# Optimization experiments

Hardware: AMD Instinct MI355X
Metric: run time of the kernel (lower is better)

Reference implementation:

```python
import jax, jax.numpy as jnp
import numpy as np
from jax import lax

B, A, H, W = 64, 8, 64, 128
T_EXP = 32
ACTION_HORIZON = 64
DS = 1.0          # reward_cfg['ds']
TEMPERATURE = 0.1 # policy_kwargs['temperature'], method='sharpen'
FOV_HALF_ANGLE_DEG = 35.0
FOV_MAX_RANGE = 100


def _build_buffers():
    # per-action 3x3 one-hot transition kernels: weight 1.0 at 'center' cell,
    # 0.0 at left/right cells (as in MaxEntIRL.__init__ with policy_method='pp')
    center = [[2, 2], [2, 1], [2, 0], [1, 2], [1, 0], [0, 2], [0, 1], [0, 0]]
    tp = np.zeros((A, 1, 3, 3), np.float32)
    for i, (r, c) in enumerate(center):
        tp[i, 0, r, c] = 1.0
    # trapezoidal FOV mask built on a (2H, W) grid, then cropped to first H rows
    rows = np.arange(2 * H, dtype=np.float32)[:, None]
    cols = np.arange(W, dtype=np.float32)[None, :]
    half = np.tan(np.deg2rad(FOV_HALF_ANGLE_DEG)) * rows
    mask = ((np.abs(cols - (W - 1) / 2.0) <= half) & (rows <= FOV_MAX_RANGE))
    fov = mask.astype(np.float32)[:H][None, None]  # (1,1,H,W)
    dyn = np.array([[-1, -1], [-1, 0], [-1, 1], [0, -1],
                    [0, 1], [1, -1], [1, 0], [1, 1]], np.int32)
    return jnp.asarray(tp), jnp.asarray(fov), jnp.asarray(dyn)


def setup_inputs() -> dict:
    key = jax.random.key(0)
    k1, k2 = jax.random.split(key)
    policy = jax.random.normal(k1, (B, A, H, W), jnp.float32)
    # expert SE(2)-like poses; only [:, :, :2, 2] translations are read.
    # Scale to [0,100) so grid cells spread over the map before clamping.
    expert = jax.random.uniform(k2, (B, T_EXP, 3, 3), jnp.float32) * 100.0
    tp, fov, dyn = _build_buffers()
    return {"policy": policy, "expert": expert, "transition_probs": tp,
            "fov_mask": fov, "dynamics": dyn, "action_horizon": ACTION_HORIZON}


def reference(policy, expert, transition_probs, fov_mask, dynamics, action_horizon):
    Bn, An, Hn, Wn = policy.shape
    n_states = Hn * Wn
    barange = jnp.arange(Bn)

    # expert poses -> clamped grid cells  (S: (B, T, 2))
    S = jnp.floor_divide(expert[:, :, :2, 2], DS).astype(jnp.int32)
    S = jnp.stack([jnp.clip(S[..., 0], 0, Hn - 1),
                   jnp.clip(S[..., 1], 0, Wn - 1)], axis=-1)

    # earliest pose inside FOV (argmax of bool gives first True, else 0)
    mask2d = fov_mask[0, 0]
    in_fov = mask2d[S[..., 0], S[..., 1]] > 0  # (B, T)
    idx0 = jnp.argmax(in_fov, axis=1)
    S0c = S[barange, idx0]     # (B, 2) start cell
    S1c = S[:, -1]             # (B, 2) terminal cell
    S0 = S0c[:, 0] * Wn + S0c[:, 1]
    S1 = S1c[:, 0] * Wn + S1c[:, 1]

    # sharpen policy over action dim (stable softmax with temperature)
    logits = (policy - jnp.max(policy, axis=1, keepdims=True)) / TEMPERATURE
    policy_2d = jax.nn.softmax(logits, axis=1)  # (B, A, H, W)

    mu0 = jnp.zeros((Bn, n_states), jnp.float32).at[barange, S0].set(1.0)

    def step(carry, _):
        prev, total = carry
        # zero_terminal_state: kill visitation mass at the terminal cell
        prev_z = prev.at[barange, S1].set(0.0)
        pm = policy_2d * prev_z.reshape(Bn, 1, Hn, Wn)  # (B, A, H, W)
        new = lax.conv_general_dilated(
            pm, transition_probs, window_strides=(1, 1),
            padding=[(1, 1), (1, 1)],
            dimension_numbers=("NCHW", "OIHW", "NCHW"),
            feature_group_count=An)
        new = jnp.sum(new, axis=1).reshape(Bn, n_states)
        return (new, total + prev_z), None

    (last, total), _ = lax.scan(step, (mu0, jnp.zeros_like(mu0)),
                                None, length=action_horizon - 1)
    mu = (total + last).reshape(Bn, Hn, Wn)

    # greedy rollout (torch runs this under no_grad)
    policy_flat = policy.reshape(Bn, An, n_states)
    most_likely_action = jnp.argmax(policy_flat, axis=1)  # (B, n_states)
    most_likely_action = lax.stop_gradient(most_likely_action)

    def roll(St, _):
        a = most_likely_action[barange, St]
        coord = jnp.stack([St // Wn, St % Wn], axis=1) + dynamics[a]
        coord = jnp.stack([jnp.clip(coord[:, 0], 0, Hn - 1),
                           jnp.clip(coord[:, 1], 0, Wn - 1)], axis=1)
        return coord[:, 0] * Wn + coord[:, 1], coord

    _, coords = lax.scan(roll, S0, None, length=action_horizon - 1)  # (T-1,B,2)
    states = jnp.concatenate([S0c[None].astype(coords.dtype), coords],
                             axis=0).transpose(1, 0, 2)  # (B, T, 2)
    bidx = jnp.broadcast_to(barange[:, None], (Bn, action_horizon))
    states_grid = jnp.zeros((Bn, Hn, Wn), jnp.float32).at[
        bidx, states[..., 0], states[..., 1]].add(1.0)
    return mu, states_grid, states
```

## Files before the change

### kernel.cpp

```cpp
#include <hip/hip_runtime.h>

#define THREADS 1024

typedef unsigned int u32;
typedef unsigned long long u64;

constexpr int BN = 64, AN = 8, HN = 64, WN = 128;
constexpr int HWN = HN * WN;
constexpr int TEXP = 32, AH = 64;
constexpr size_t LDS_BYTES = (size_t)AN * HWN * 2;

constexpr int GYc[8] = { 1, 1, 1, 0, 0, -1, -1, -1 };
constexpr int GXc[8] = { 1, 0, -1, 1, -1, 1, 0, -1 };

typedef _Float16 h2 __attribute__((ext_vector_type(2)));
union U { u32 u; h2 p; _Float16 h[2]; };

__device__ __forceinline__ h2  H(u32 x) { U t; t.u = x; return t.p; }
__device__ __forceinline__ u32 Bc(h2 x) { U t; t.p = x; return t.u; }

__device__ __forceinline__ u32 ab16(u32 hi, u32 lo) {
    return (u32)((((u64)hi << 32) | lo) >> 16);
}
__device__ __forceinline__ u32 wsr1(u32 x) {
    return (u32)__builtin_amdgcn_update_dpp(0, (int)x, 0x138, 0xf, 0xf, true);
}
__device__ __forceinline__ u32 wsl1(u32 x) {
    return (u32)__builtin_amdgcn_update_dpp(0, (int)x, 0x130, 0xf, 0xf, true);
}
__device__ __forceinline__ u32 shL(u32 d) { return ab16(d, wsr1(d)); }
__device__ __forceinline__ u32 shR(u32 d) { return ab16(wsl1(d), d); }

extern "C" __global__ __launch_bounds__(THREADS)
void maxent_fused(const float* __restrict__ policy,
                  const float* __restrict__ expert,
                  const float* __restrict__ fovm,
                  const int*   __restrict__ dyn,
                  float* __restrict__ out)
{
    (void)dyn;
    extern __shared__ char smem[];
    const int tid  = threadIdx.x;
    const int lane = tid & 63;
    const bool isScan = blockIdx.x < BN;
    const int b = isScan ? (int)blockIdx.x : (int)blockIdx.x - BN;

    int Sr = 0, Sc = 0; bool infov = false;
    if (lane < TEXP) {
        float e0 = expert[b * (TEXP * 9) + lane * 9 + 2];
        float e1 = expert[b * (TEXP * 9) + lane * 9 + 5];
        int r = (int)floorf(e0); r = r < 0 ? 0 : (r > HN - 1 ? HN - 1 : r);
        int c = (int)floorf(e1); c = c < 0 ? 0 : (c > WN - 1 ? WN - 1 : c);
        Sr = r; Sc = c;
        infov = fovm[r * WN + c] > 0.0f;
    }
    unsigned long long fmask = __ballot(infov);
    int idx0 = fmask ? (__ffsll(fmask) - 1) : 0;
    const int S0r = __shfl(Sr, idx0), S0c = __shfl(Sc, idx0);
    const int S1r = __shfl(Sr, TEXP - 1), S1c = __shfl(Sc, TEXP - 1);
    const bool S0eqS1 = (S0r == S1r) && (S0c == S1c);

    if (isScan) {
        _Float16* Pl = (_Float16*)smem;

        const float* pb = policy + (size_t)b * AN * HWN;
        #pragma unroll
        for (int kk = 0; kk < 2; ++kk) {
            const int pix = (kk * THREADS + tid) * 4;
            float v[8][4];
            float m[4] = {-3.4e38f, -3.4e38f, -3.4e38f, -3.4e38f};
            #pragma unroll
            for (int a = 0; a < 8; ++a) {
                float4 f = *(const float4*)(pb + a * HWN + pix);
                v[a][0] = f.x; v[a][1] = f.y; v[a][2] = f.z; v[a][3] = f.w;
                m[0] = fmaxf(m[0], f.x); m[1] = fmaxf(m[1], f.y);
                m[2] = fmaxf(m[2], f.z); m[3] = fmaxf(m[3], f.w);
            }
            float s[4] = {0.f, 0.f, 0.f, 0.f};
            #pragma unroll
            for (int a = 0; a < 8; ++a)
                #pragma unroll
                for (int j = 0; j < 4; ++j) { v[a][j] = __expf((v[a][j] - m[j]) * 10.0f); s[j] += v[a][j]; }
            float inv[4];
            #pragma unroll
            for (int j = 0; j < 4; ++j) inv[j] = 1.0f / s[j];
            #pragma unroll
            for (int a = 0; a < 8; ++a) {
                u32 lo = (u32)__builtin_bit_cast(unsigned short, (_Float16)(v[a][0] * inv[0]))
                       | ((u32)__builtin_bit_cast(unsigned short, (_Float16)(v[a][1] * inv[1])) << 16);
                u32 hi = (u32)__builtin_bit_cast(unsigned short, (_Float16)(v[a][2] * inv[2]))
                       | ((u32)__builtin_bit_cast(unsigned short, (_Float16)(v[a][3] * inv[3])) << 16);
                uint2 pk2; pk2.x = lo; pk2.y = hi;
                *(uint2*)(Pl + a * HWN + pix) = pk2;
            }
        }
        __syncthreads();

        const int w = tid >> 6;
        const int rbase = 4 * w;

        u32 pa[8][4];
        #pragma unroll
        for (int a = 0; a < 8; ++a) {
            const int gy = GYc[a], gx = GXc[a];
            #pragma unroll
            for (int r = 0; r < 4; ++r) {
                const int sr = rbase + r + gy;
                u32 d = 0;
                if (sr >= 0 && sr < HN)
                    d = *(const u32*)(Pl + a * HWN + sr * WN + 2 * lane);
                pa[a][r] = (gx == 0) ? d : ((gx == 1) ? shR(d) : shL(d));
            }
        }
        __syncthreads();

        u32* hx  = (u32*)smem;
        u32* flg = hx + 4096;
        for (int i = tid; i < 4096 + 256; i += THREADS) hx[i] = 0;

        u32 x[6], zm[4];
        #pragma unroll
        for (int r = 0; r < 4; ++r) {
            const int gr = rbase + r;
            x[1 + r] = (!S0eqS1 && gr == S0r && (S0c >> 1) == lane)
                         ? ((S0c & 1) ? 0x3C000000u : 0x00003C00u) : 0u;
            zm[r] = ~0u;
            if (gr == S1r && (S1c >> 1) == lane)
                zm[r] = (S1c & 1) ? 0x0000FFFFu : 0xFFFF0000u;
        }
        x[0] = 0; x[5] = 0;

        int t0 = rbase - S0r; { int t1 = S0r - (rbase + 3); if (t1 > t0) t0 = t1; }
        const int t_act = (t0 > 1) ? (t0 - 1) : 0;

        __syncthreads();
        hx[(2 * w + 0) * 64 + lane] = x[1];
        hx[(2 * w + 1) * 64 + lane] = x[4];
        if (lane == 0) flg[w * 16] = (u32)t_act;
        __syncthreads();

        u32 t16[4], nn[4];
        float tot[8];
        #pragma unroll
        for (int r = 0; r < 4; ++r) { t16[r] = 0; nn[r] = 0; }
        #pragma unroll
        for (int k = 0; k < 8; ++k) tot[k] = 0.f;

        const int rdT = (2 * w - 1) * 64 + lane;
        const int rdD = (2 * w + 2) * 64 + lane;
        const int wr0 = (2 * w + 0) * 64 + lane;
        const int wr3 = (2 * w + 1) * 64 + lane;
        u32* fL = flg + (w - 1) * 16;
        u32* fR = flg + (w + 1) * 16;
        u32* fme = flg + w * 16;

        for (int it = t_act; it < AH - 1; ++it) {
            const int pb_ = (it & 1) << 11;
            const int wb_ = 2048 - pb_;

            if (w > 0)
                while (__hip_atomic_load(fL, __ATOMIC_ACQUIRE, __HIP_MEMORY_SCOPE_WORKGROUP) < (u32)it)
                    __builtin_amdgcn_s_sleep(1);
            if (w < 15)
                while (__hip_atomic_load(fR, __ATOMIC_ACQUIRE, __HIP_MEMORY_SCOPE_WORKGROUP) < (u32)it)
                    __builtin_amdgcn_s_sleep(1);

            const u32 hT = (w > 0)  ? hx[pb_ + rdT] : 0u;
            const u32 hD = (w < 15) ? hx[pb_ + rdD] : 0u;

            #pragma unroll
            for (int r = 0; r < 4; ++r) t16[r] = Bc(H(t16[r]) + H(x[1 + r]));

            u32 L[6], R[6];
            #pragma unroll
            for (int i = 1; i <= 4; ++i) { L[i] = shL(x[i]); R[i] = shR(x[i]); }

            u32 ns[4];
            constexpr int RO[4] = {1, 2, 0, 3};
            #pragma unroll
            for (int ri = 0; ri < 4; ++ri) {
                const int r = RO[ri];
                const u32 cm1 = (r == 0) ? hT      : x[r];
                const u32 lm1 = (r == 0) ? shL(hT) : L[r];
                const u32 rm1 = (r == 0) ? shR(hT) : R[r];
                const u32 cp1 = (r == 3) ? hD      : x[r + 2];
                const u32 lp1 = (r == 3) ? shL(hD) : L[r + 2];
                const u32 rp1 = (r == 3) ? shR(hD) : R[r + 2];
                h2 acc0 =  H(pa[0][r]) * H(rp1);
                acc0 += H(pa[1][r]) * H(cp1);
                acc0 += H(pa[2][r]) * H(lp1);
                acc0 += H(pa[3][r]) * H(R[r + 1]);
                h2 acc1 =  H(pa[4][r]) * H(L[r + 1]);
                acc1 += H(pa[5][r]) * H(rm1);
                acc1 += H(pa[6][r]) * H(cm1);
                acc1 += H(pa[7][r]) * H(lm1);
                const u32 un = Bc(acc0 + acc1);
                nn[r] = un;
                ns[r] = un & zm[r];
            }
            #pragma unroll
            for (int r = 0; r < 4; ++r) x[1 + r] = ns[r];

            hx[wb_ + wr0] = x[1];
            hx[wb_ + wr3] = x[4];
            __hip_atomic_store(fme, (u32)(it + 1), __ATOMIC_RELEASE, __HIP_MEMORY_SCOPE_WORKGROUP);

            if ((it & 3) == 3 || it == AH - 2) {
                #pragma unroll
                for (int r = 0; r < 4; ++r) {
                    tot[2*r]   += (float)H(t16[r]).x;
                    tot[2*r+1] += (float)H(t16[r]).y;
                    t16[r] = 0;
                }
            }
        }

        #pragma unroll
        for (int r = 0; r < 4; ++r) {
            float2 f;
            f.x = tot[2*r]   + (float)H(nn[r]).x;
            f.y = tot[2*r+1] + (float)H(nn[r]).y;
            *(float2*)(out + (size_t)b * HWN + (rbase + r) * WN + 2 * lane) = f;
        }

    } else {
        short* amap = (short*)smem;
        float* grid = (float*)(smem + 16384);
        const float* pb = policy + (size_t)b * AN * HWN;
        #pragma unroll
        for (int c = 0; c < 2; ++c) {
            const int pix = (c * THREADS + tid) * 4;
            float4 f0 = *(const float4*)(pb + pix);
            float b0 = f0.x, b1 = f0.y, b2 = f0.z, b3 = f0.w;
            int a0 = 0, a1 = 0, a2 = 0, a3 = 0;
            #pragma unroll
            for (int a = 1; a < 8; ++a) {
                float4 f = *(const float4*)(pb + a * HWN + pix);
                if (f.x > b0) { b0 = f.x; a0 = a; }
                if (f.y > b1) { b1 = f.y; a1 = a; }
                if (f.z > b2) { b2 = f.z; a2 = a; }
                if (f.w > b3) { b3 = f.w; a3 = a; }
            }
            uint2 pk2;
            pk2.x = (u32)a0 | ((u32)a1 << 16);
            pk2.y = (u32)a2 | ((u32)a3 << 16);
            *(uint2*)(amap + pix) = pk2;
        }
        for (int i = tid; i < HWN; i += THREADS) grid[i] = 0.f;
        __syncthreads();

        if (tid == 0) {
            float* so = out + 2 * (size_t)HWN * BN + b * (AH * 2);
            int cr = S0r, cc = S0c;
            so[0] = (float)cr; so[1] = (float)cc;
            grid[cr * WN + cc] += 1.0f;
            for (int t = 1; t < AH; ++t) {
                const int a = amap[cr * WN + cc];
                const int dr = (a < 3) ? -1 : ((a < 5) ? 0 : 1);
                int dc;
                if (a < 3) dc = a - 1;
                else if (a == 3) dc = -1;
                else if (a == 4) dc = 1;
                else dc = a - 6;
                cr += dr; cc += dc;
                cr = cr < 0 ? 0 : (cr > HN - 1 ? HN - 1 : cr);
                cc = cc < 0 ? 0 : (cc > WN - 1 ? WN - 1 : cc);
                so[t * 2] = (float)cr; so[t * 2 + 1] = (float)cc;
                grid[cr * WN + cc] += 1.0f;
            }
        }
        __syncthreads();
        float* sg = out + (size_t)HWN * BN + b * HWN;
        for (int i = tid; i < HWN; i += THREADS) sg[i] = grid[i];
    }
}

extern "C" void kernel_launch(void* const* d_in, const int* in_sizes, int n_in,
                              void* d_out, int out_size, void* d_ws, size_t ws_size,
                              hipStream_t stream) {
    const float* policy = (const float*)d_in[0];
    const float* expert = (const float*)d_in[1];
    const float* fovm   = (const float*)d_in[3];
    const int*   dyn    = (const int*)d_in[4];
    float* out = (float*)d_out;

    (void)hipFuncSetAttribute((const void*)maxent_fused,
                              hipFuncAttributeMaxDynamicSharedMemorySize,
                              (int)LDS_BYTES);
    hipLaunchKernelGGL(maxent_fused, dim3(2 * BN), dim3(THREADS), LDS_BYTES, stream,
                       policy, expert, fovm, dyn, out);
}
```

Baseline: 53.32 us.

## Precompute halo-independent boundary-row partials to shorten inter-wave critical path

Boundary rows 0 and 3 are now split into a partial sum that uses only the wave's own rows, computed at the end of the previous iteration, plus a halo-dependent remainder. After the flag wait, each wave finishes and publishes its edge rows first, then computes the interior rows. This shortens the latency between a neighbour's flag and this wave's own flag release. The spin-wait also drops s_sleep, which reacts faster but adds LDS polling pressure. The changed accumulation order in fp16 may shift rounding slightly.

```diff
diff --git a/kernel.cpp b/kernel.cpp
--- a/kernel.cpp
+++ b/kernel.cpp
@@ -154,16 +154,28 @@
         u32* fR = flg + (w + 1) * 16;
         u32* fme = flg + w * 16;
 
+        u32 L[6], R[6], part0, part3;
+        #pragma unroll
+        for (int i = 1; i <= 4; ++i) { L[i] = shL(x[i]); R[i] = shR(x[i]); }
+        {
+            h2 p0 = H(pa[0][0]) * H(R[2]);  p0 += H(pa[1][0]) * H(x[2]);
+            p0 += H(pa[2][0]) * H(L[2]);    p0 += H(pa[3][0]) * H(R[1]);
+            p0 += H(pa[4][0]) * H(L[1]);
+            part0 = Bc(p0);
+            h2 p3 = H(pa[3][3]) * H(R[4]);  p3 += H(pa[4][3]) * H(L[4]);
+            p3 += H(pa[5][3]) * H(R[3]);    p3 += H(pa[6][3]) * H(x[3]);
+            p3 += H(pa[7][3]) * H(L[3]);
+            part3 = Bc(p3);
+        }
+
         for (int it = t_act; it < AH - 1; ++it) {
             const int pb_ = (it & 1) << 11;
             const int wb_ = 2048 - pb_;
 
             if (w > 0)
-                while (__hip_atomic_load(fL, __ATOMIC_ACQUIRE, __HIP_MEMORY_SCOPE_WORKGROUP) < (u32)it)
-                    __builtin_amdgcn_s_sleep(1);
+                while (__hip_atomic_load(fL, __ATOMIC_ACQUIRE, __HIP_MEMORY_SCOPE_WORKGROUP) < (u32)it) {}
             if (w < 15)
-                while (__hip_atomic_load(fR, __ATOMIC_ACQUIRE, __HIP_MEMORY_SCOPE_WORKGROUP) < (u32)it)
-                    __builtin_amdgcn_s_sleep(1);
+                while (__hip_atomic_load(fR, __ATOMIC_ACQUIRE, __HIP_MEMORY_SCOPE_WORKGROUP) < (u32)it) {}
 
             const u32 hT = (w > 0)  ? hx[pb_ + rdT] : 0u;
             const u32 hD = (w < 15) ? hx[pb_ + rdD] : 0u;
@@ -171,39 +183,43 @@
             #pragma unroll
             for (int r = 0; r < 4; ++r) t16[r] = Bc(H(t16[r]) + H(x[1 + r]));
 
-            u32 L[6], R[6];
+            h2 a0 = H(part0) + H(pa[5][0]) * H(shR(hT));
+            a0 += H(pa[6][0]) * H(hT);
+            a0 += H(pa[7][0]) * H(shL(hT));
+            h2 a3 = H(part3) + H(pa[0][3]) * H(shR(hD));
+            a3 += H(pa[1][3]) * H(hD);
+            a3 += H(pa[2][3]) * H(shL(hD));
+            const u32 n0 = Bc(a0), n3 = Bc(a3);
+            const u32 x1n = n0 & zm[0], x4n = n3 & zm[3];
+            hx[wb_ + wr0] = x1n;
+            hx[wb_ + wr3] = x4n;
+            __hip_atomic_store(fme, (u32)(it + 1), __ATOMIC_RELEASE, __HIP_MEMORY_SCOPE_WORKGROUP);
+
+            h2 a1 = H(pa[0][1]) * H(R[3]);  a1 += H(pa[1][1]) * H(x[3]);
+            a1 += H(pa[2][1]) * H(L[3]);    a1 += H(pa[3][1]) * H(R[2]);
+            a1 += H(pa[4][1]) * H(L[2]);    a1 += H(pa[5][1]) * H(R[1]);
+            a1 += H(pa[6][1]) * H(x[1]);    a1 += H(pa[7][1]) * H(L[1]);
+            h2 a2 = H(pa[0][2]) * H(R[4]);  a2 += H(pa[1][2]) * H(x[4]);
+            a2 += H(pa[2][2]) * H(L[4]);    a2 += H(pa[3][2]) * H(R[3]);
+            a2 += H(pa[4][2]) * H(L[3]);    a2 += H(pa[5][2]) * H(R[2]);
+            a2 += H(pa[6][2]) * H(x[2]);    a2 += H(pa[7][2]) * H(L[2]);
+            const u32 n1 = Bc(a1), n2 = Bc(a2);
+
+            nn[0] = n0; nn[1] = n1; nn[2] = n2; nn[3] = n3;
+            x[1] = x1n; x[2] = n1 & zm[1]; x[3] = n2 & zm[2]; x[4] = x4n;
+
             #pragma unroll
             for (int i = 1; i <= 4; ++i) { L[i] = shL(x[i]); R[i] = shR(x[i]); }
-
-            u32 ns[4];
-            constexpr int RO[4] = {1, 2, 0, 3};
-            #pragma unroll
-            for (int ri = 0; ri < 4; ++ri) {
-                const int r = RO[ri];
-                const u32 cm1 = (r == 0) ? hT      : x[r];
-                const u32 lm1 = (r == 0) ? shL(hT) : L[r];
-                const u32 rm1 = (r == 0) ? shR(hT) : R[r];
-                const u32 cp1 = (r == 3) ? hD      : x[r + 2];
-                const u32 lp1 = (r == 3) ? shL(hD) : L[r + 2];
-                const u32 rp1 = (r == 3) ? shR(hD) : R[r + 2];
-                h2 acc0 =  H(pa[0][r]) * H(rp1);
-                acc0 += H(pa[1][r]) * H(cp1);
-                acc0 += H(pa[2][r]) * H(lp1);
-                acc0 += H(pa[3][r]) * H(R[r + 1]);
-                h2 acc1 =  H(pa[4][r]) * H(L[r + 1]);
-                acc1 += H(pa[5][r]) * H(rm1);
-                acc1 += H(pa[6][r]) * H(cm1);
-                acc1 += H(pa[7][r]) * H(lm1);
-                const u32 un = Bc(acc0 + acc1);
-                nn[r] = un;
-                ns[r] = un & zm[r];
-            }
-            #pragma unroll
-            for (int r = 0; r < 4; ++r) x[1 + r] = ns[r];
-
-            hx[wb_ + wr0] = x[1];
-            hx[wb_ + wr3] = x[4];
-            __hip_atomic_store(fme, (u32)(it + 1), __ATOMIC_RELEASE, __HIP_MEMORY_SCOPE_WORKGROUP);
+            {
+                h2 p0 = H(pa[0][0]) * H(R[2]);  p0 += H(pa[1][0]) * H(x[2]);
+                p0 += H(pa[2][0]) * H(L[2]);    p0 += H(pa[3][0]) * H(R[1]);
+                p0 += H(pa[4][0]) * H(L[1]);
+                part0 = Bc(p0);
+                h2 p3 = H(pa[3][3]) * H(R[4]);  p3 += H(pa[4][3]) * H(L[4]);
+                p3 += H(pa[5][3]) * H(R[3]);    p3 += H(pa[6][3]) * H(x[3]);
+                p3 += H(pa[7][3]) * H(L[3]);
+                part3 = Bc(p3);
+            }
 
             if ((it & 3) == 3 || it == AH - 2) {
                 #pragma unroll
```

Result: no change. 52.99 us (-0.6%).

## Pack two batch scans per workgroup with eight rows per wavefront

Applied to the files above, without the earlier changes.

Each scan workgroup now handles two batch elements, with 8 wavefronts per batch and 8 rows per wave instead of 16 waves at 4 rows each. The grid shrinks from 128 to 96 blocks. The goal is fewer halo exchanges and flag spins per row and less inter-wave sync in the recurrence. In exchange each workgroup does its softmax preprocessing twice in sequence, and the unrolled loop holds twice as many registers (pa is 8x8), which raises register pressure.

```diff
diff --git a/kernel.cpp b/kernel.cpp
--- a/kernel.cpp
+++ b/kernel.cpp
@@ -3,11 +3,13 @@
 #define THREADS 1024
 
 typedef unsigned int u32;
+typedef unsigned short u16;
 typedef unsigned long long u64;
 
 constexpr int BN = 64, AN = 8, HN = 64, WN = 128;
 constexpr int HWN = HN * WN;
 constexpr int TEXP = 32, AH = 64;
+constexpr int SCANB = 32;
 constexpr size_t LDS_BYTES = (size_t)AN * HWN * 2;
 
 constexpr int GYc[8] = { 1, 1, 1, 0, 0, -1, -1, -1 };
@@ -42,8 +44,11 @@
     extern __shared__ char smem[];
     const int tid  = threadIdx.x;
     const int lane = tid & 63;
-    const bool isScan = blockIdx.x < BN;
-    const int b = isScan ? (int)blockIdx.x : (int)blockIdx.x - BN;
+    const bool isScan = blockIdx.x < SCANB;
+    const int wv16 = tid >> 6;
+    const int g    = wv16 >> 3;
+    const int lw   = wv16 & 7;
+    const int b = isScan ? ((int)blockIdx.x * 2 + g) : ((int)blockIdx.x - SCANB);
 
     int Sr = 0, Sc = 0; bool infov = false;
     if (lane < TEXP) {
@@ -62,65 +67,67 @@
 
     if (isScan) {
         _Float16* Pl = (_Float16*)smem;
-
-        const float* pb = policy + (size_t)b * AN * HWN;
-        #pragma unroll
-        for (int kk = 0; kk < 2; ++kk) {
-            const int pix = (kk * THREADS + tid) * 4;
-            float v[8][4];
-            float m[4] = {-3.4e38f, -3.4e38f, -3.4e38f, -3.4e38f};
-            #pragma unroll
-            for (int a = 0; a < 8; ++a) {
-                float4 f = *(const float4*)(pb + a * HWN + pix);
-                v[a][0] = f.x; v[a][1] = f.y; v[a][2] = f.z; v[a][3] = f.w;
-                m[0] = fmaxf(m[0], f.x); m[1] = fmaxf(m[1], f.y);
-                m[2] = fmaxf(m[2], f.z); m[3] = fmaxf(m[3], f.w);
-            }
-            float s[4] = {0.f, 0.f, 0.f, 0.f};
-            #pragma unroll
-            for (int a = 0; a < 8; ++a)
-                #pragma unroll
-                for (int j = 0; j < 4; ++j) { v[a][j] = __expf((v[a][j] - m[j]) * 10.0f); s[j] += v[a][j]; }
-            float inv[4];
-            #pragma unroll
-            for (int j = 0; j < 4; ++j) inv[j] = 1.0f / s[j];
-            #pragma unroll
-            for (int a = 0; a < 8; ++a) {
-                u32 lo = (u32)__builtin_bit_cast(unsigned short, (_Float16)(v[a][0] * inv[0]))
-                       | ((u32)__builtin_bit_cast(unsigned short, (_Float16)(v[a][1] * inv[1])) << 16);
-                u32 hi = (u32)__builtin_bit_cast(unsigned short, (_Float16)(v[a][2] * inv[2]))
-                       | ((u32)__builtin_bit_cast(unsigned short, (_Float16)(v[a][3] * inv[3])) << 16);
-                uint2 pk2; pk2.x = lo; pk2.y = hi;
-                *(uint2*)(Pl + a * HWN + pix) = pk2;
-            }
-        }
-        __syncthreads();
-
-        const int w = tid >> 6;
-        const int rbase = 4 * w;
-
-        u32 pa[8][4];
-        #pragma unroll
-        for (int a = 0; a < 8; ++a) {
-            const int gy = GYc[a], gx = GXc[a];
-            #pragma unroll
-            for (int r = 0; r < 4; ++r) {
-                const int sr = rbase + r + gy;
-                u32 d = 0;
-                if (sr >= 0 && sr < HN)
-                    d = *(const u32*)(Pl + a * HWN + sr * WN + 2 * lane);
-                pa[a][r] = (gx == 0) ? d : ((gx == 1) ? shR(d) : shL(d));
-            }
-        }
-        __syncthreads();
+        const int rbase = 8 * lw;
+        u32 pa[8][8];
+
+        for (int gg = 0; gg < 2; ++gg) {
+            const int bb = (int)blockIdx.x * 2 + gg;
+            const float* pb = policy + (size_t)bb * AN * HWN;
+            #pragma unroll
+            for (int kk = 0; kk < 2; ++kk) {
+                const int pix = (kk * THREADS + tid) * 4;
+                float v[8][4];
+                float m[4] = {-3.4e38f, -3.4e38f, -3.4e38f, -3.4e38f};
+                #pragma unroll
+                for (int a = 0; a < 8; ++a) {
+                    float4 f = *(const float4*)(pb + a * HWN + pix);
+                    v[a][0] = f.x; v[a][1] = f.y; v[a][2] = f.z; v[a][3] = f.w;
+                    m[0] = fmaxf(m[0], f.x); m[1] = fmaxf(m[1], f.y);
+                    m[2] = fmaxf(m[2], f.z); m[3] = fmaxf(m[3], f.w);
+                }
+                float s[4] = {0.f, 0.f, 0.f, 0.f};
+                #pragma unroll
+                for (int a = 0; a < 8; ++a)
+                    #pragma unroll
+                    for (int j = 0; j < 4; ++j) { v[a][j] = __expf((v[a][j] - m[j]) * 10.0f); s[j] += v[a][j]; }
+                float inv[4];
+                #pragma unroll
+                for (int j = 0; j < 4; ++j) inv[j] = 1.0f / s[j];
+                #pragma unroll
+                for (int a = 0; a < 8; ++a) {
+                    u32 lo = (u32)__builtin_bit_cast(u16, (_Float16)(v[a][0] * inv[0]))
+                           | ((u32)__builtin_bit_cast(u16, (_Float16)(v[a][1] * inv[1])) << 16);
+                    u32 hi = (u32)__builtin_bit_cast(u16, (_Float16)(v[a][2] * inv[2]))
+                           | ((u32)__builtin_bit_cast(u16, (_Float16)(v[a][3] * inv[3])) << 16);
+                    uint2 pk2; pk2.x = lo; pk2.y = hi;
+                    *(uint2*)(Pl + a * HWN + pix) = pk2;
+                }
+            }
+            __syncthreads();
+            if (g == gg) {
+                #pragma unroll
+                for (int a = 0; a < 8; ++a) {
+                    const int gy = GYc[a], gx = GXc[a];
+                    #pragma unroll
+                    for (int r = 0; r < 8; ++r) {
+                        const int sr = rbase + r + gy;
+                        u32 d = 0;
+                        if (sr >= 0 && sr < HN)
+                            d = *(const u32*)(Pl + a * HWN + sr * WN + 2 * lane);
+                        pa[a][r] = (gx == 0) ? d : ((gx == 1) ? shR(d) : shL(d));
+                    }
+                }
+            }
+            __syncthreads();
+        }
 
         u32* hx  = (u32*)smem;
         u32* flg = hx + 4096;
         for (int i = tid; i < 4096 + 256; i += THREADS) hx[i] = 0;
 
-        u32 x[6], zm[4];
-        #pragma unroll
-        for (int r = 0; r < 4; ++r) {
+        u32 x[10], zm[8];
+        #pragma unroll
+        for (int r = 0; r < 8; ++r) {
             const int gr = rbase + r;
             x[1 + r] = (!S0eqS1 && gr == S0r && (S0c >> 1) == lane)
                          ? ((S0c & 1) ? 0x3C000000u : 0x00003C00u) : 0u;
@@ -128,64 +135,65 @@
             if (gr == S1r && (S1c >> 1) == lane)
                 zm[r] = (S1c & 1) ? 0x0000FFFFu : 0xFFFF0000u;
         }
-        x[0] = 0; x[5] = 0;
-
-        int t0 = rbase - S0r; { int t1 = S0r - (rbase + 3); if (t1 > t0) t0 = t1; }
+        x[0] = 0; x[9] = 0;
+
+        int t0 = rbase - S0r; { int t1 = S0r - (rbase + 7); if (t1 > t0) t0 = t1; }
         const int t_act = (t0 > 1) ? (t0 - 1) : 0;
 
         __syncthreads();
-        hx[(2 * w + 0) * 64 + lane] = x[1];
-        hx[(2 * w + 1) * 64 + lane] = x[4];
-        if (lane == 0) flg[w * 16] = (u32)t_act;
+        const int gb = g * 2048;
+        hx[gb + (2 * lw + 0) * 64 + lane] = x[1];
+        hx[gb + (2 * lw + 1) * 64 + lane] = x[8];
+        if (lane == 0) flg[(g * 8 + lw) * 16] = (u32)t_act;
         __syncthreads();
 
-        u32 t16[4], nn[4];
-        float tot[8];
-        #pragma unroll
-        for (int r = 0; r < 4; ++r) { t16[r] = 0; nn[r] = 0; }
-        #pragma unroll
-        for (int k = 0; k < 8; ++k) tot[k] = 0.f;
-
-        const int rdT = (2 * w - 1) * 64 + lane;
-        const int rdD = (2 * w + 2) * 64 + lane;
-        const int wr0 = (2 * w + 0) * 64 + lane;
-        const int wr3 = (2 * w + 1) * 64 + lane;
-        u32* fL = flg + (w - 1) * 16;
-        u32* fR = flg + (w + 1) * 16;
-        u32* fme = flg + w * 16;
+        u32 t16[8], nn[8];
+        float tot[16];
+        #pragma unroll
+        for (int r = 0; r < 8; ++r) { t16[r] = 0; nn[r] = 0; }
+        #pragma unroll
+        for (int k = 0; k < 16; ++k) tot[k] = 0.f;
+
+        const int rdT = (2 * lw - 1) * 64 + lane;
+        const int rdD = (2 * lw + 2) * 64 + lane;
+        const int wr0 = (2 * lw + 0) * 64 + lane;
+        const int wr7 = (2 * lw + 1) * 64 + lane;
+        u32* fL = flg + (g * 8 + lw - 1) * 16;
+        u32* fR = flg + (g * 8 + lw + 1) * 16;
+        u32* fme = flg + (g * 8 + lw) * 16;
 
         for (int it = t_act; it < AH - 1; ++it) {
-            const int pb_ = (it & 1) << 11;
-            const int wb_ = 2048 - pb_;
-
-            if (w > 0)
+            const int pb_ = gb + ((it & 1) << 10);
+            const int wb_ = gb + (1024 - ((it & 1) << 10));
+
+            if (lw > 0)
                 while (__hip_atomic_load(fL, __ATOMIC_ACQUIRE, __HIP_MEMORY_SCOPE_WORKGROUP) < (u32)it)
                     __builtin_amdgcn_s_sleep(1);
-            if (w < 15)
+            if (lw < 7)
                 while (__hip_atomic_load(fR, __ATOMIC_ACQUIRE, __HIP_MEMORY_SCOPE_WORKGROUP) < (u32)it)
                     __builtin_amdgcn_s_sleep(1);
 
-            const u32 hT = (w > 0)  ? hx[pb_ + rdT] : 0u;
-            const u32 hD = (w < 15) ? hx[pb_ + rdD] : 0u;
-
-            #pragma unroll
-            for (int r = 0; r < 4; ++r) t16[r] = Bc(H(t16[r]) + H(x[1 + r]));
-
-            u32 L[6], R[6];
-            #pragma unroll
-            for (int i = 1; i <= 4; ++i) { L[i] = shL(x[i]); R[i] = shR(x[i]); }
-
-            u32 ns[4];
-            constexpr int RO[4] = {1, 2, 0, 3};
-            #pragma unroll
-            for (int ri = 0; ri < 4; ++ri) {
+            const u32 hT = (lw > 0) ? hx[pb_ + rdT] : 0u;
+            const u32 hD = (lw < 7) ? hx[pb_ + rdD] : 0u;
+
+            #pragma unroll
+            for (int r = 0; r < 8; ++r) t16[r] = Bc(H(t16[r]) + H(x[1 + r]));
+
+            u32 L[9], R[9];
+            #pragma unroll
+            for (int i = 1; i <= 8; ++i) { L[i] = shL(x[i]); R[i] = shR(x[i]); }
+
+            u32 ns[8];
+            constexpr int RO[8] = {1, 2, 3, 4, 5, 6, 0, 7};
+            #pragma unroll
+            for (int ri = 0; ri < 8; ++ri) {
                 const int r = RO[ri];
                 const u32 cm1 = (r == 0) ? hT      : x[r];
                 const u32 lm1 = (r == 0) ? shL(hT) : L[r];
                 const u32 rm1 = (r == 0) ? shR(hT) : R[r];
-                const u32 cp1 = (r == 3) ? hD      : x[r + 2];
-                const u32 lp1 = (r == 3) ? shL(hD) : L[r + 2];
-                const u32 rp1 = (r == 3) ? shR(hD) : R[r + 2];
+                const u32 cp1 = (r == 7) ? hD      : x[r + 2];
+                const u32 lp1 = (r == 7) ? shL(hD) : L[r + 2];
+                const u32 rp1 = (r == 7) ? shR(hD) : R[r + 2];
                 h2 acc0 =  H(pa[0][r]) * H(rp1);
                 acc0 += H(pa[1][r]) * H(cp1);
                 acc0 += H(pa[2][r]) * H(lp1);
@@ -199,15 +207,15 @@
                 ns[r] = un & zm[r];
             }
             #pragma unroll
-            for (int r = 0; r < 4; ++r) x[1 + r] = ns[r];
+            for (int r = 0; r < 8; ++r) x[1 + r] = ns[r];
 
             hx[wb_ + wr0] = x[1];
-            hx[wb_ + wr3] = x[4];
+            hx[wb_ + wr7] = x[8];
             __hip_atomic_store(fme, (u32)(it + 1), __ATOMIC_RELEASE, __HIP_MEMORY_SCOPE_WORKGROUP);
 
             if ((it & 3) == 3 || it == AH - 2) {
                 #pragma unroll
-                for (int r = 0; r < 4; ++r) {
+                for (int r = 0; r < 8; ++r) {
                     tot[2*r]   += (float)H(t16[r]).x;
                     tot[2*r+1] += (float)H(t16[r]).y;
                     t16[r] = 0;
@@ -216,7 +224,7 @@
         }
 
         #pragma unroll
-        for (int r = 0; r < 4; ++r) {
+        for (int r = 0; r < 8; ++r) {
             float2 f;
             f.x = tot[2*r]   + (float)H(nn[r]).x;
             f.y = tot[2*r+1] + (float)H(nn[r]).y;
@@ -287,6 +295,6 @@
     (void)hipFuncSetAttribute((const void*)maxent_fused,
                               hipFuncAttributeMaxDynamicSharedMemorySize,
                               (int)LDS_BYTES);
-    hipLaunchKernelGGL(maxent_fused, dim3(2 * BN), dim3(THREADS), LDS_BYTES, stream,
+    hipLaunchKernelGGL(maxent_fused, dim3(SCANB + BN), dim3(THREADS), LDS_BYTES, stream,
                        policy, expert, fovm, dyn, out);
 }
```

Result: slower. 99.14 us (+85.9%).
